# Kernel tuning notes

Measured on AMD Instinct MI355X. Metric: run time of the kernel, lower is better.

The kernel has to match this reference:

```python
import jax, jax.numpy as jnp
import numpy as np
import math

D_MODEL = 256
NUM_SLOTS = 128
RANK = 32
STEPS = 6
VOCAB = 32000
SEQ = 512
BATCH = 8
LN_EPS = 1e-5


def setup_inputs() -> dict:
    key = jax.random.key(0)
    ks = jax.random.split(key, 16)
    std = 0.02
    inp = {
        "input_ids": jax.random.randint(ks[0], (BATCH, SEQ), 0, VOCAB),
        "attention_mask": jnp.ones((BATCH, SEQ), dtype=jnp.int32),
        "token_emb": jax.random.normal(ks[1], (VOCAB, D_MODEL), jnp.float32) * std,
        "pos_emb": jax.random.normal(ks[2], (SEQ, D_MODEL), jnp.float32) * std,
        "H": jax.random.normal(ks[3], (NUM_SLOTS, D_MODEL), jnp.float32) / math.sqrt(D_MODEL),
        "W_source": jax.random.normal(ks[4], (NUM_SLOTS, NUM_SLOTS, D_MODEL, RANK), jnp.float32) * std,
        "W_target": jax.random.normal(ks[5], (NUM_SLOTS, NUM_SLOTS, RANK, D_MODEL), jnp.float32) * std,
        "Wq_in": jax.random.normal(ks[6], (D_MODEL, D_MODEL), jnp.float32) / math.sqrt(D_MODEL),
        "Wk_slots": jax.random.normal(ks[7], (D_MODEL, D_MODEL), jnp.float32) / math.sqrt(D_MODEL),
        "Wv_in": jax.random.normal(ks[8], (D_MODEL, D_MODEL), jnp.float32) / math.sqrt(D_MODEL),
        "Wq_out": jax.random.normal(ks[9], (D_MODEL, D_MODEL), jnp.float32) / math.sqrt(D_MODEL),
        "Wk_fin": jax.random.normal(ks[10], (D_MODEL, D_MODEL), jnp.float32) / math.sqrt(D_MODEL),
        "Wv_fin": jax.random.normal(ks[11], (D_MODEL, D_MODEL), jnp.float32) / math.sqrt(D_MODEL),
        "W_out_proj": jax.random.normal(ks[12], (VOCAB, D_MODEL), jnp.float32) / math.sqrt(D_MODEL),
        "ln_scale": jnp.ones((STEPS, D_MODEL), jnp.float32),
        "ln_bias": jnp.zeros((STEPS, D_MODEL), jnp.float32),
    }
    return inp


def _layernorm(x, g, b):
    mu = jnp.mean(x, axis=-1, keepdims=True)
    var = jnp.var(x, axis=-1, keepdims=True)
    return (x - mu) / jnp.sqrt(var + LN_EPS) * g + b


def _forward(input_ids, attention_mask, token_emb, pos_emb, H, W_source, W_target,
             Wq_in, Wk_slots, Wv_in, Wq_out, Wk_fin, Wv_fin, W_out_proj, ln_scale, ln_bias):
    B, L = input_ids.shape
    scale = 1.0 / math.sqrt(D_MODEL)
    # embeddings (dropout is identity in eval)
    X = token_emb[input_ids] + pos_emb[jnp.arange(L)][None]  # (B,L,D)
    # compress: input tokens -> slots
    Q_in = X @ Wq_in.T                      # (B,L,D)
    K_sl = H @ Wk_slots.T                   # (S,D)
    V_in = X @ Wv_in.T                      # (B,L,D)
    A = jax.nn.softmax(Q_in @ K_sl.T * scale, axis=-1)  # (B,L,S)
    m = attention_mask.astype(A.dtype)[..., None]
    A = A * m
    A = A / (jnp.sum(A, axis=1, keepdims=True) + 1e-8)
    IR = jnp.einsum('bls,bld->bsd', A, V_in)            # (B,S,D)
    H_state = H[None] + IR                               # (B,S,D)

    off_diag = (1.0 - jnp.eye(NUM_SLOTS, dtype=H_state.dtype))  # (S,S)

    def step(h, lnp):
        g, b = lnp
        # bilinear slot-to-slot influence; contract directly, no (B,S,S,D) expand of h
        inter = jnp.einsum('bid,ijdr->bijr', h, W_source)        # (B,S,S,R)
        out = jnp.einsum('bijr,ijrd->bijd', inter, W_target)     # (B,S,S,D)
        infl = jnp.einsum('bijd,ij->bjd', out, off_diag)         # mask diag + sum over i
        h = _layernorm(h + jax.nn.relu(infl), g, b)
        return h, None

    H_state, _ = jax.lax.scan(step, H_state, (ln_scale, ln_bias))

    # expand: slots -> tokens
    Q_out = X @ Wq_out.T                   # (B,L,D)
    K_f = H_state @ Wk_fin.T               # (B,S,D)
    V_f = H_state @ Wv_fin.T               # (B,S,D)
    A2 = jax.nn.softmax(jnp.einsum('bld,bsd->bls', Q_out, K_f) * scale, axis=-1)
    Y = jnp.einsum('bls,bsd->bld', A2, V_f)
    logits = Y @ W_out_proj.T              # (B,L,V)
    return logits


def reference(input_ids, attention_mask, token_emb, pos_emb, H, W_source, W_target,
              Wq_in, Wk_slots, Wv_in, Wq_out, Wk_fin, Wv_fin, W_out_proj, ln_scale, ln_bias):
    return _forward(input_ids, attention_mask, token_emb, pos_emb, H, W_source, W_target,
                    Wq_in, Wk_slots, Wv_in, Wq_out, Wk_fin, Wv_fin, W_out_proj, ln_scale, ln_bias)
```

## Files before the change

### kernel.cpp

```cpp
#include <hip/hip_runtime.h>
#include <hip/hip_bf16.h>
#include <math.h>

#define D_MODEL 256
#define NUM_SLOTS 128
#define RANK 32
#define N_STEPS 6
#define VOCAB 32000
#define SEQ 512
#define BATCH 8
#define NTOK (BATCH*SEQ)
#define LN_EPS 1e-5f
#define SM_SCALE 0.0625f
#define IGROUPS 8
#define IPG (NUM_SLOTS/IGROUPS)

typedef __attribute__((ext_vector_type(8))) short bf16x8;
typedef __attribute__((ext_vector_type(8))) _Float16 f16x8;
typedef __attribute__((ext_vector_type(4))) float f32x4;

#define GLD_LDS16(g, l) __builtin_amdgcn_global_load_lds( \
    (const __attribute__((address_space(1))) unsigned int*)(g), \
    (__attribute__((address_space(3))) unsigned int*)(l), 16, 0, 0)

__device__ inline unsigned pk2(float a, float b) {
    auto v = __builtin_amdgcn_cvt_pkrtz(a, b);
    union { decltype(v) x; unsigned u; } c;
    c.x = v;
    return c.u;
}
__device__ inline unsigned short f2h(float x) {
    union { _Float16 h; unsigned short u; } c;
    c.h = (_Float16)x;
    return c.u;
}

__global__ __launch_bounds__(256) void k_gemm_nt(const float* __restrict__ A,
        const float* __restrict__ B, float* __restrict__ C, int M, int N, int K) {
    __shared__ float As[32][64];
    __shared__ float Bs[32][64];
    int bm = blockIdx.x * 64, bn = blockIdx.y * 64;
    int t = threadIdx.x;
    int tm = (t & 15) * 4, tn = (t >> 4) * 4;
    float acc[4][4] = {};
    for (int k0 = 0; k0 < K; k0 += 32) {
        #pragma unroll
        for (int r = 0; r < 8; ++r) {
            int idx = r*256 + t;
            int m = idx >> 5, k = idx & 31;
            As[k][m] = A[(size_t)(bm+m)*K + k0 + k];
        }
        #pragma unroll
        for (int r = 0; r < 8; ++r) {
            int idx = r*256 + t;
            int n = idx >> 5, k = idx & 31;
            Bs[k][n] = B[(size_t)(bn+n)*K + k0 + k];
        }
        __syncthreads();
        #pragma unroll
        for (int k = 0; k < 32; ++k) {
            float4 a4 = *(const float4*)&As[k][tm];
            float4 b4 = *(const float4*)&Bs[k][tn];
            float a[4] = {a4.x,a4.y,a4.z,a4.w};
            float b[4] = {b4.x,b4.y,b4.z,b4.w};
            #pragma unroll
            for (int i = 0; i < 4; ++i)
                #pragma unroll
                for (int jj = 0; jj < 4; ++jj)
                    acc[i][jj] += a[i]*b[jj];
        }
        __syncthreads();
    }
    #pragma unroll
    for (int i = 0; i < 4; ++i) {
        float4 v = make_float4(acc[i][0],acc[i][1],acc[i][2],acc[i][3]);
        *(float4*)&C[(size_t)(bm+tm+i)*N + bn+tn] = v;
    }
}

__global__ __launch_bounds__(256) void k_gemm3e(const int* __restrict__ ids,
        const float* __restrict__ tok, const float* __restrict__ pos,
        const float* __restrict__ B0, const float* __restrict__ B1,
        const float* __restrict__ B2, float* __restrict__ C0,
        float* __restrict__ C1, float* __restrict__ C2) {
    const int K = D_MODEL, N = D_MODEL;
    const float* B = blockIdx.z == 0 ? B0 : (blockIdx.z == 1 ? B1 : B2);
    float* C = blockIdx.z == 0 ? C0 : (blockIdx.z == 1 ? C1 : C2);
    __shared__ float As[32][64];
    __shared__ float Bs[32][64];
    __shared__ int sid[64];
    int bm = blockIdx.x * 64, bn = blockIdx.y * 64;
    int t = threadIdx.x;
    if (t < 64) sid[t] = ids[bm + t];
    __syncthreads();
    int tm = (t & 15) * 4, tn = (t >> 4) * 4;
    float acc[4][4] = {};
    for (int k0 = 0; k0 < K; k0 += 32) {
        #pragma unroll
        for (int r = 0; r < 8; ++r) {
            int idx = r*256 + t;
            int m = idx >> 5, k = idx & 31;
            int gm = bm + m;
            As[k][m] = tok[(size_t)sid[m]*K + k0 + k] + pos[(gm & (SEQ-1))*K + k0 + k];
        }
        #pragma unroll
        for (int r = 0; r < 8; ++r) {
            int idx = r*256 + t;
            int n = idx >> 5, k = idx & 31;
            Bs[k][n] = B[(size_t)(bn+n)*K + k0 + k];
        }
        __syncthreads();
        #pragma unroll
        for (int k = 0; k < 32; ++k) {
            float4 a4 = *(const float4*)&As[k][tm];
            float4 b4 = *(const float4*)&Bs[k][tn];
            float a[4] = {a4.x,a4.y,a4.z,a4.w};
            float b[4] = {b4.x,b4.y,b4.z,b4.w};
            #pragma unroll
            for (int i = 0; i < 4; ++i)
                #pragma unroll
                for (int jj = 0; jj < 4; ++jj)
                    acc[i][jj] += a[i]*b[jj];
        }
        __syncthreads();
    }
    #pragma unroll
    for (int i = 0; i < 4; ++i) {
        float4 v = make_float4(acc[i][0],acc[i][1],acc[i][2],acc[i][3]);
        *(float4*)&C[(size_t)(bm+tm+i)*N + bn+tn] = v;
    }
}

__global__ __launch_bounds__(128) void k_attn1(const float* __restrict__ Qin,
        const float* __restrict__ Ksl, const int* __restrict__ mask,
        float* __restrict__ A) {
    int bl = blockIdx.x;
    int s = threadIdx.x;
    __shared__ float q[D_MODEL];
    __shared__ float red[128];
    q[s]       = Qin[(size_t)bl*D_MODEL + s];
    q[s + 128] = Qin[(size_t)bl*D_MODEL + s + 128];
    __syncthreads();
    const float* kr = Ksl + (size_t)s*D_MODEL;
    float acc = 0.f;
    #pragma unroll 8
    for (int d = 0; d < D_MODEL; ++d) acc += q[d]*kr[d];
    acc *= SM_SCALE;
    red[s] = acc; __syncthreads();
    for (int o = 64; o > 0; o >>= 1) { if (s < o) red[s] = fmaxf(red[s], red[s+o]); __syncthreads(); }
    float mx = red[0]; __syncthreads();
    float e = expf(acc - mx);
    red[s] = e; __syncthreads();
    for (int o = 64; o > 0; o >>= 1) { if (s < o) red[s] += red[s+o]; __syncthreads(); }
    float sum = red[0];
    float m = (float)mask[bl];
    A[(size_t)bl*NUM_SLOTS + s] = e / sum * m;
}

__global__ __launch_bounds__(256) void k_split16(const float* __restrict__ in,
        unsigned short* __restrict__ o, int n4) {
    int i = blockIdx.x*256 + threadIdx.x;
    if (i >= n4) return;
    float4 v = ((const float4*)in)[i];
    ushort4 h;
    h.x = f2h(v.x); h.y = f2h(v.y); h.z = f2h(v.z); h.w = f2h(v.w);
    ((ushort4*)o)[i] = h;
}

__global__ __launch_bounds__(256) void k_logits(
        const unsigned short* __restrict__ Ahg,
        const unsigned short* __restrict__ Bhg, float* __restrict__ C) {
    __shared__ unsigned short lds[2*8192];
    int bm = blockIdx.x * 128, bn = blockIdx.y * 128;
    int t = threadIdx.x;
    int w = t >> 6, l = t & 63;
    int wr = w >> 1, wc = w & 1;
    int lr = l & 15, lk = l >> 4;
    f32x4 acc[4][4];
    #pragma unroll
    for (int mi = 0; mi < 4; ++mi)
        #pragma unroll
        for (int ni = 0; ni < 4; ++ni)
            acc[mi][ni] = (f32x4){0.f,0.f,0.f,0.f};

    for (int kc = 0; kc < 4; ++kc) {
        if (kc) __syncthreads();
        #pragma unroll
        for (int i = 0; i < 4; ++i) {
            int c = t + i*256;
            int row = c >> 3, c8 = c & 7;
            size_t ga = (size_t)(bm+row)*256 + kc*64 + c8*8;
            size_t gb = (size_t)(bn+row)*256 + kc*64 + c8*8;
            GLD_LDS16(Ahg + ga, &lds[c*8]);
            GLD_LDS16(Bhg + gb, &lds[8192 + c*8]);
        }
        __syncthreads();
        #pragma unroll
        for (int s = 0; s < 2; ++s) {
            f16x8 ah[4], bh[4];
            #pragma unroll
            for (int mi = 0; mi < 4; ++mi) {
                int off = (wr*64 + mi*16 + lr)*64 + s*32 + lk*8;
                ah[mi] = *(const f16x8*)&lds[off];
            }
            #pragma unroll
            for (int ni = 0; ni < 4; ++ni) {
                int off = (wc*64 + ni*16 + lr)*64 + s*32 + lk*8;
                bh[ni] = *(const f16x8*)&lds[8192 + off];
            }
            #pragma unroll
            for (int mi = 0; mi < 4; ++mi)
                #pragma unroll
                for (int ni = 0; ni < 4; ++ni)
                    acc[mi][ni] = __builtin_amdgcn_mfma_f32_16x16x32_f16(ah[mi], bh[ni], acc[mi][ni], 0, 0, 0);
        }
    }
    #pragma unroll
    for (int mi = 0; mi < 4; ++mi)
        #pragma unroll
        for (int ni = 0; ni < 4; ++ni) {
            int col = bn + wc*64 + ni*16 + lr;
            #pragma unroll
            for (int r = 0; r < 4; ++r) {
                int row = bm + wr*64 + mi*16 + lk*4 + r;
                C[(size_t)row*VOCAB + col] = acc[mi][ni][r];
            }
        }
}

__global__ __launch_bounds__(256) void k_ir(const float* __restrict__ A,
        const float* __restrict__ V, const float* __restrict__ H,
        float* __restrict__ Hs, unsigned short* __restrict__ Hs16) {
    int bs = blockIdx.x; int b = bs >> 7; int s = bs & 127;
    int d = threadIdx.x;
    const float* Ab = A + (size_t)b*SEQ*NUM_SLOTS + s;
    const float* Vb = V + (size_t)b*SEQ*D_MODEL + d;
    float a0 = 0.f, a1 = 0.f, a2 = 0.f, a3 = 0.f;
    float s0 = 0.f, s1 = 0.f, s2 = 0.f, s3 = 0.f;
    for (int l = 0; l < SEQ; l += 4) {
        float w0 = Ab[(size_t)(l+0)*NUM_SLOTS];
        float w1 = Ab[(size_t)(l+1)*NUM_SLOTS];
        float w2 = Ab[(size_t)(l+2)*NUM_SLOTS];
        float w3 = Ab[(size_t)(l+3)*NUM_SLOTS];
        a0 += w0 * Vb[(size_t)(l+0)*D_MODEL];
        a1 += w1 * Vb[(size_t)(l+1)*D_MODEL];
        a2 += w2 * Vb[(size_t)(l+2)*D_MODEL];
        a3 += w3 * Vb[(size_t)(l+3)*D_MODEL];
        s0 += w0; s1 += w1; s2 += w2; s3 += w3;
    }
    float asum = (s0+s1) + (s2+s3) + 1e-8f;
    float acc = (a0+a1) + (a2+a3);
    float v = H[s*D_MODEL + d] + acc / asum;
    Hs[(size_t)bs*D_MODEL + d] = v;
    Hs16[(size_t)bs*D_MODEL + d] = f2h(v);
}

__global__ __launch_bounds__(256) void k_convert(const float* __restrict__ Ws,
        const float* __restrict__ Wt, unsigned short* __restrict__ WF) {
    int i = blockIdx.x, j = blockIdx.y, z = blockIdx.z;
    int t = threadIdx.x, w = t >> 6, l = t & 63;
    __shared__ float lds[4*1056];
    float* lw = &lds[w*1056];
    size_t sBase = ((size_t)i*128 + j)*8192;
    size_t pOut = ((size_t)j*128 + i)*16384;
    int g = l >> 4, c = l & 15;
    if (z < 2) {
        int ks = z*4 + w;
        const float4* s4 = (const float4*)(Ws + sBase) + ks*256;
        #pragma unroll
        for (int q = 0; q < 4; ++q) {
            int idx = q*64 + l;
            float4 v = s4[idx];
            *(float4*)&lw[(idx>>3)*33 + 4*(idx&7)] = v;
        }
        asm volatile("s_waitcnt lgkmcnt(0)" ::: "memory");
        bool diag = (i == j);
        #pragma unroll
        for (int mt = 0; mt < 2; ++mt) {
            union { f16x8 v; } o;
            #pragma unroll
            for (int e = 0; e < 8; ++e) {
                float f = diag ? 0.f : lw[(g*8 + e)*33 + mt*16 + c];
                o.v[e] = (_Float16)f;
            }
            *(f16x8*)(WF + pOut + (size_t)((ks*2 + mt)*64 + l)*8) = o.v;
        }
    } else {
        int p0 = (z - 2)*8 + w*2;
        const float4* s4 = (const float4*)(Wt + sBase);
        #pragma unroll
        for (int q = 0; q < 4; ++q) {
            int idx = q*64 + l;
            int r = idx >> 3, c8 = idx & 7;
            float4 v = s4[r*64 + p0*4 + c8];
            *(float4*)&lw[r*33 + 4*c8] = v;
        }
        asm volatile("s_waitcnt lgkmcnt(0)" ::: "memory");
        #pragma unroll
        for (int dn = 0; dn < 2; ++dn) {
            int nt = p0 + dn;
            union { f16x8 v; } o;
            #pragma unroll
            for (int e = 0; e < 8; ++e)
                o.v[e] = (_Float16)lw[(g*8 + e)*33 + dn*16 + c];
            *(f16x8*)(WF + pOut + 8192 + (size_t)(nt*64 + l)*8) = o.v;
        }
    }
}

__global__ __launch_bounds__(256, 4) void k_pairs_mfma(const unsigned short* __restrict__ h16,
        const unsigned short* __restrict__ WF, float* __restrict__ part) {
    __shared__ unsigned short lds[2*10240];
    int j = blockIdx.x, g = blockIdx.y;
    int t = threadIdx.x, w = t >> 6, l = t & 63;
    int lg = l >> 4, c = l & 15;
    const unsigned short* pbase = WF + ((size_t)j*128 + g*16)*16384;

    {
        const unsigned short* src = pbase;
        #pragma unroll
        for (int q = 0; q < 4; ++q)
            GLD_LDS16(src + (size_t)(q*256 + t)*8, &lds[(q*256 + t)*8]);
        const unsigned short* hsrc = h16 + ((size_t)(t&7)*NUM_SLOTS + g*16)*D_MODEL + (t>>3)*8;
        GLD_LDS16(hsrc, &lds[8192 + t*8]);
    }
    __builtin_amdgcn_sched_barrier(0);
    f16x8 bqn[4];
    #pragma unroll
    for (int nt = 0; nt < 4; ++nt)
        bqn[nt] = *(const f16x8*)(pbase + 8192 + (size_t)((w*4+nt)*64 + l)*8);
    __builtin_amdgcn_sched_barrier(0);

    f32x4 acc[4];
    #pragma unroll
    for (int nt = 0; nt < 4; ++nt) acc[nt] = (f32x4){0.f,0.f,0.f,0.f};
    f16x8 hzero;
    #pragma unroll
    for (int e = 0; e < 8; ++e) hzero[e] = (_Float16)0.f;

    #pragma unroll 2
    for (int ii = 0; ii < 16; ++ii) {
        int cur = ii & 1;
        asm volatile("s_waitcnt vmcnt(4) lgkmcnt(0)" ::: "memory");
        __builtin_amdgcn_s_barrier();
        __builtin_amdgcn_sched_barrier(0);
        if (ii < 15) {
            const unsigned short* src = pbase + (size_t)(ii+1)*16384;
            unsigned short* dst = &lds[(cur^1)*10240];
            #pragma unroll
            for (int q = 0; q < 4; ++q)
                GLD_LDS16(src + (size_t)(q*256 + t)*8, dst + (size_t)(q*256 + t)*8);
            const unsigned short* hsrc = h16 + ((size_t)(t&7)*NUM_SLOTS + (g*16+ii+1))*D_MODEL + (t>>3)*8;
            GLD_LDS16(hsrc, dst + 8192 + (size_t)t*8);
        }
        __builtin_amdgcn_sched_barrier(0);
        f16x8 bq[4];
        #pragma unroll
        for (int nt = 0; nt < 4; ++nt) bq[nt] = bqn[nt];
        if (ii < 15) {
            const unsigned short* bp = pbase + (size_t)(ii+1)*16384 + 8192;
            #pragma unroll
            for (int nt = 0; nt < 4; ++nt)
                bqn[nt] = *(const f16x8*)(bp + (size_t)((w*4+nt)*64 + l)*8);
        }
        const unsigned short* buf = &lds[cur*10240];
        f32x4 d1[2];
        d1[0] = (f32x4){0.f,0.f,0.f,0.f};
        d1[1] = (f32x4){0.f,0.f,0.f,0.f};
        #pragma unroll
        for (int ks = 0; ks < 8; ++ks) {
            f16x8 a0 = *(const f16x8*)(buf + (size_t)((ks*2+0)*64 + l)*8);
            f16x8 a1 = *(const f16x8*)(buf + (size_t)((ks*2+1)*64 + l)*8);
            f16x8 hv = *(const f16x8*)(buf + 8192 + (size_t)(((ks*4+lg)*8 + (c&7)))*8);
            f16x8 hb = (c < 8) ? hv : hzero;
            d1[0] = __builtin_amdgcn_mfma_f32_16x16x32_f16(a0, hb, d1[0], 0, 0, 0);
            d1[1] = __builtin_amdgcn_mfma_f32_16x16x32_f16(a1, hb, d1[1], 0, 0, 0);
        }
        unsigned q0 = pk2(d1[0][0], d1[0][1]);
        unsigned q1 = pk2(d1[0][2], d1[0][3]);
        unsigned s0 = pk2(d1[1][0], d1[1][1]);
        unsigned s1 = pk2(d1[1][2], d1[1][3]);
        int srcLo = 32*(lg & 1) + c;
        int srcHi = srcLo + 16;
        unsigned a0s = (unsigned)__shfl((int)q0, srcLo, 64);
        unsigned a1s = (unsigned)__shfl((int)q1, srcLo, 64);
        unsigned a2s = (unsigned)__shfl((int)q0, srcHi, 64);
        unsigned a3s = (unsigned)__shfl((int)q1, srcHi, 64);
        unsigned b0s = (unsigned)__shfl((int)s0, srcLo, 64);
        unsigned b1s = (unsigned)__shfl((int)s1, srcLo, 64);
        unsigned b2s = (unsigned)__shfl((int)s0, srcHi, 64);
        unsigned b3s = (unsigned)__shfl((int)s1, srcHi, 64);
        bool himt = ((lg >> 1) & 1);
        union { unsigned u[4]; f16x8 v; } A2u;
        A2u.u[0] = himt ? b0s : a0s;
        A2u.u[1] = himt ? b1s : a1s;
        A2u.u[2] = himt ? b2s : a2s;
        A2u.u[3] = himt ? b3s : a3s;
        #pragma unroll
        for (int nt = 0; nt < 4; ++nt)
            acc[nt] = __builtin_amdgcn_mfma_f32_16x16x32_f16(A2u.v, bq[nt], acc[nt], 0, 0, 0);
    }
    if (lg < 2) {
        #pragma unroll
        for (int nt = 0; nt < 4; ++nt) {
            int d = (w*4 + nt)*16 + c;
            #pragma unroll
            for (int r = 0; r < 4; ++r) {
                int b = lg*4 + r;
                part[(((size_t)g*BATCH + b)*NUM_SLOTS + j)*D_MODEL + d] = acc[nt][r];
            }
        }
    }
}

__global__ __launch_bounds__(256) void k_ln(float* __restrict__ h,
        unsigned short* __restrict__ h16, const float* __restrict__ part,
        const float* __restrict__ gma, const float* __restrict__ bta) {
    int bj = blockIdx.x;
    int t = threadIdx.x;
    int b = bj >> 7, j = bj & 127;
    __shared__ float red[256];
    float v = 0.f;
    #pragma unroll
    for (int g = 0; g < IGROUPS; ++g)
        v += part[(((size_t)g*BATCH + b)*NUM_SLOTS + j)*D_MODEL + t];
    float x = h[(size_t)bj*D_MODEL + t] + fmaxf(v, 0.f);
    red[t] = x; __syncthreads();
    for (int o = 128; o > 0; o >>= 1) { if (t < o) red[t] += red[t+o]; __syncthreads(); }
    float mu = red[0] * (1.0f/D_MODEL); __syncthreads();
    float dx = x - mu;
    red[t] = dx*dx; __syncthreads();
    for (int o = 128; o > 0; o >>= 1) { if (t < o) red[t] += red[t+o]; __syncthreads(); }
    float var = red[0] * (1.0f/D_MODEL);
    float outv = dx * rsqrtf(var + LN_EPS) * gma[t] + bta[t];
    h[(size_t)bj*D_MODEL + t] = outv;
    h16[(size_t)bj*D_MODEL + t] = f2h(outv);
}

__global__ __launch_bounds__(256) void k_kfvf(const float* __restrict__ A,
        const float* __restrict__ B0, const float* __restrict__ B1,
        float* __restrict__ C0, float* __restrict__ C1) {
    const int K = D_MODEL, N = D_MODEL;
    const float* B = blockIdx.z == 0 ? B0 : B1;
    float* C = blockIdx.z == 0 ? C0 : C1;
    __shared__ float As[32][64];
    __shared__ float Bs[32][64];
    int bm = blockIdx.x * 64, bn = blockIdx.y * 64;
    int t = threadIdx.x;
    int tm = (t & 15) * 4, tn = (t >> 4) * 4;
    float acc[4][4] = {};
    for (int k0 = 0; k0 < K; k0 += 32) {
        #pragma unroll
        for (int r = 0; r < 8; ++r) {
            int idx = r*256 + t;
            int m = idx >> 5, k = idx & 31;
            As[k][m] = A[(size_t)(bm+m)*K + k0 + k];
        }
        #pragma unroll
        for (int r = 0; r < 8; ++r) {
            int idx = r*256 + t;
            int n = idx >> 5, k = idx & 31;
            Bs[k][n] = B[(size_t)(bn+n)*K + k0 + k];
        }
        __syncthreads();
        #pragma unroll
        for (int k = 0; k < 32; ++k) {
            float4 a4 = *(const float4*)&As[k][tm];
            float4 b4 = *(const float4*)&Bs[k][tn];
            float a[4] = {a4.x,a4.y,a4.z,a4.w};
            float b[4] = {b4.x,b4.y,b4.z,b4.w};
            #pragma unroll
            for (int i = 0; i < 4; ++i)
                #pragma unroll
                for (int jj = 0; jj < 4; ++jj)
                    acc[i][jj] += a[i]*b[jj];
        }
        __syncthreads();
    }
    #pragma unroll
    for (int i = 0; i < 4; ++i) {
        float4 v = make_float4(acc[i][0],acc[i][1],acc[i][2],acc[i][3]);
        *(float4*)&C[(size_t)(bm+tm+i)*N + bn+tn] = v;
    }
}

__global__ __launch_bounds__(256) void k_attn2y(const float* __restrict__ Q,
        const float* __restrict__ Kf, const float* __restrict__ Vf,
        unsigned short* __restrict__ Yh) {
    int bl = blockIdx.x; int b = bl / SEQ;
    int t = threadIdx.x;
    __shared__ float q[D_MODEL];
    __shared__ float prt[2][128];
    __shared__ float a[128];
    __shared__ float red[128];
    q[t] = Q[(size_t)bl*D_MODEL + t];
    __syncthreads();
    int s = t & 127, hf = t >> 7;
    const float* kf = Kf + ((size_t)b*NUM_SLOTS + s)*D_MODEL + hf*128;
    float accp = 0.f;
    #pragma unroll 8
    for (int d = 0; d < 128; ++d) accp += q[hf*128 + d]*kf[d];
    prt[hf][s] = accp;
    __syncthreads();
    float v = 0.f;
    if (t < 128) { v = (prt[0][t] + prt[1][t]) * SM_SCALE; red[t] = v; }
    __syncthreads();
    for (int o = 64; o > 0; o >>= 1) { if (t < o) red[t] = fmaxf(red[t], red[t+o]); __syncthreads(); }
    float mx = red[0]; __syncthreads();
    if (t < 128) { float e = expf(v - mx); a[t] = e; red[t] = e; }
    __syncthreads();
    for (int o = 64; o > 0; o >>= 1) { if (t < o) red[t] += red[t+o]; __syncthreads(); }
    float inv = 1.0f / red[0];
    __syncthreads();
    const float* vf = Vf + (size_t)b*NUM_SLOTS*D_MODEL + t;
    float y0 = 0.f, y1 = 0.f, y2 = 0.f, y3 = 0.f;
    #pragma unroll
    for (int s2 = 0; s2 < NUM_SLOTS; s2 += 4) {
        y0 += a[s2+0]*vf[(size_t)(s2+0)*D_MODEL];
        y1 += a[s2+1]*vf[(size_t)(s2+1)*D_MODEL];
        y2 += a[s2+2]*vf[(size_t)(s2+2)*D_MODEL];
        y3 += a[s2+3]*vf[(size_t)(s2+3)*D_MODEL];
    }
    float y = ((y0+y1) + (y2+y3)) * inv;
    Yh[(size_t)bl*D_MODEL + t] = f2h(y);
}

extern "C" void kernel_launch(void* const* d_in, const int* in_sizes, int n_in,
                              void* d_out, int out_size, void* d_ws, size_t ws_size,
                              hipStream_t stream) {
    const int*   ids    = (const int*)d_in[0];
    const int*   amask  = (const int*)d_in[1];
    const float* tok    = (const float*)d_in[2];
    const float* pos    = (const float*)d_in[3];
    const float* Hin    = (const float*)d_in[4];
    const float* Ws     = (const float*)d_in[5];
    const float* Wt     = (const float*)d_in[6];
    const float* Wq_in  = (const float*)d_in[7];
    const float* Wk_sl  = (const float*)d_in[8];
    const float* Wv_in  = (const float*)d_in[9];
    const float* Wq_out = (const float*)d_in[10];
    const float* Wk_fin = (const float*)d_in[11];
    const float* Wv_fin = (const float*)d_in[12];
    const float* Wop    = (const float*)d_in[13];
    const float* lnsc   = (const float*)d_in[14];
    const float* lnbs   = (const float*)d_in[15];
    float* out = (float*)d_out;

    const size_t WF_USH = (size_t)16384 * 16384;
    unsigned short* WF = (unsigned short*)d_ws;
    float* ws = (float*)(WF + WF_USH);

    float* X    = ws;
    float* Qin  = X    + (size_t)NTOK*D_MODEL;
    float* Vin  = Qin  + (size_t)NTOK*D_MODEL;
    float* Ksl  = Vin  + (size_t)NTOK*D_MODEL;
    float* Asc  = Ksl  + (size_t)NUM_SLOTS*D_MODEL;
    float* csp  = Asc  + (size_t)NTOK*NUM_SLOTS;
    float* Hst  = csp  + (size_t)BATCH*8*NUM_SLOTS;
    float* part = Hst  + (size_t)BATCH*NUM_SLOTS*D_MODEL;
    float* Qout = part + (size_t)IGROUPS*BATCH*NUM_SLOTS*D_MODEL;
    float* Kf   = Qout + (size_t)NTOK*D_MODEL;
    float* Vf   = Kf   + (size_t)BATCH*NUM_SLOTS*D_MODEL;
    float* A2   = Vf   + (size_t)BATCH*NUM_SLOTS*D_MODEL;
    float* Yb   = A2   + (size_t)NTOK*NUM_SLOTS;
    unsigned short* Yh = (unsigned short*)(Yb + (size_t)NTOK*D_MODEL);
    unsigned short* Yl = Yh + (size_t)NTOK*D_MODEL;
    unsigned short* Wf16 = Yl + (size_t)NTOK*D_MODEL;
    unsigned short* Hst16 = Wf16 + (size_t)VOCAB*D_MODEL;

    k_convert<<<dim3(128, 128, 4), 256, 0, stream>>>(Ws, Wt, WF);
    k_split16<<<(VOCAB*D_MODEL/4 + 255)/256, 256, 0, stream>>>(Wop, Wf16, VOCAB*D_MODEL/4);

    k_gemm3e<<<dim3(NTOK/64, 4, 3), 256, 0, stream>>>(ids, tok, pos,
            Wq_in, Wv_in, Wq_out, Qin, Vin, Qout);
    k_gemm_nt<<<dim3(2, 4), 256, 0, stream>>>(Hin, Wk_sl, Ksl, NUM_SLOTS, D_MODEL, D_MODEL);
    k_attn1<<<NTOK, 128, 0, stream>>>(Qin, Ksl, amask, Asc);
    k_ir<<<BATCH*NUM_SLOTS, 256, 0, stream>>>(Asc, Vin, Hin, Hst, Hst16);
    for (int st = 0; st < N_STEPS; ++st) {
        k_pairs_mfma<<<dim3(NUM_SLOTS, IGROUPS), 256, 0, stream>>>(Hst16, WF, part);
        k_ln<<<BATCH*NUM_SLOTS, 256, 0, stream>>>(Hst, Hst16, part, lnsc + st*D_MODEL, lnbs + st*D_MODEL);
    }
    k_kfvf<<<dim3(BATCH*NUM_SLOTS/64, 4, 2), 256, 0, stream>>>(Hst, Wk_fin, Wv_fin, Kf, Vf);
    k_attn2y<<<NTOK, 256, 0, stream>>>(Qout, Kf, Vf, Yh);
    k_logits<<<dim3(NTOK/128, VOCAB/128), 256, 0, stream>>>(Yh, Wf16, out);
}
```

Before: 1.423 ms.

## Fuse front-end kernels with pair-weight conversion blocks to overlap independent work

The large W_source/W_target fp16 conversion and the W_out_proj split are no longer separate launches. Their blocks are appended to the front-end kernels (QKV projection, slot key GEMM, slot attention, slot aggregation), so the bandwidth-bound conversion runs alongside the small dependent front-end stages. This aims to fill idle CUs during those small kernels and remove launch gaps. The slot attention kernel also now uses 256 threads that split the dot product in half. In exchange the front kernels carry extra branching and a larger shared footprint, and the conversion is split across four launches that must add up to the full 65536 blocks.

```diff
diff --git a/kernel.cpp b/kernel.cpp
--- a/kernel.cpp
+++ b/kernel.cpp
@@ -13,7 +13,15 @@
 #define LN_EPS 1e-5f
 #define SM_SCALE 0.0625f
 #define IGROUPS 8
-#define IPG (NUM_SLOTS/IGROUPS)
+
+#define CB_A 0
+#define NC_A 15360
+#define CB_B (CB_A + NC_A)
+#define NC_B 11776
+#define CB_C (CB_B + NC_B)
+#define NC_C 19200
+#define CB_D (CB_C + NC_C)
+#define NC_D 19200
 
 typedef __attribute__((ext_vector_type(8))) short bf16x8;
 typedef __attribute__((ext_vector_type(8))) _Float16 f16x8;
@@ -35,12 +43,81 @@
     return c.u;
 }
 
-__global__ __launch_bounds__(256) void k_gemm_nt(const float* __restrict__ A,
-        const float* __restrict__ B, float* __restrict__ C, int M, int N, int K) {
-    __shared__ float As[32][64];
-    __shared__ float Bs[32][64];
-    int bm = blockIdx.x * 64, bn = blockIdx.y * 64;
-    int t = threadIdx.x;
+__device__ __forceinline__ void dev_convert(int cb, int t, float* ldsAll,
+        const float* __restrict__ Ws, const float* __restrict__ Wt,
+        unsigned short* __restrict__ WF) {
+    int z = cb >> 14, i = (cb >> 7) & 127, j = cb & 127;
+    int w = t >> 6, l = t & 63;
+    float* lw = &ldsAll[w*1056];
+    size_t sBase = ((size_t)i*128 + j)*8192;
+    size_t pOut = ((size_t)j*128 + i)*16384;
+    int g = l >> 4, c = l & 15;
+    if (z < 2) {
+        int ks = z*4 + w;
+        const float4* s4 = (const float4*)(Ws + sBase) + ks*256;
+        #pragma unroll
+        for (int q = 0; q < 4; ++q) {
+            int idx = q*64 + l;
+            float4 v = s4[idx];
+            *(float4*)&lw[(idx>>3)*33 + 4*(idx&7)] = v;
+        }
+        asm volatile("s_waitcnt lgkmcnt(0)" ::: "memory");
+        bool diag = (i == j);
+        #pragma unroll
+        for (int mt = 0; mt < 2; ++mt) {
+            union { f16x8 v; } o;
+            #pragma unroll
+            for (int e = 0; e < 8; ++e) {
+                float f = diag ? 0.f : lw[(g*8 + e)*33 + mt*16 + c];
+                o.v[e] = (_Float16)f;
+            }
+            *(f16x8*)(WF + pOut + (size_t)((ks*2 + mt)*64 + l)*8) = o.v;
+        }
+    } else {
+        int p0 = (z - 2)*8 + w*2;
+        const float4* s4 = (const float4*)(Wt + sBase);
+        #pragma unroll
+        for (int q = 0; q < 4; ++q) {
+            int idx = q*64 + l;
+            int r = idx >> 3, c8 = idx & 7;
+            float4 v = s4[r*64 + p0*4 + c8];
+            *(float4*)&lw[r*33 + 4*c8] = v;
+        }
+        asm volatile("s_waitcnt lgkmcnt(0)" ::: "memory");
+        #pragma unroll
+        for (int dn = 0; dn < 2; ++dn) {
+            int nt = p0 + dn;
+            union { f16x8 v; } o;
+            #pragma unroll
+            for (int e = 0; e < 8; ++e)
+                o.v[e] = (_Float16)lw[(g*8 + e)*33 + dn*16 + c];
+            *(f16x8*)(WF + pOut + 8192 + (size_t)(nt*64 + l)*8) = o.v;
+        }
+    }
+}
+
+__global__ __launch_bounds__(256) void k_front_a(const int* __restrict__ ids,
+        const float* __restrict__ tok, const float* __restrict__ pos,
+        const float* __restrict__ B0, const float* __restrict__ B1,
+        const float* __restrict__ B2, float* __restrict__ C0,
+        float* __restrict__ C1, float* __restrict__ C2,
+        const float* __restrict__ Ws, const float* __restrict__ Wt,
+        unsigned short* __restrict__ WF) {
+    __shared__ float smem[4352];
+    int bid = blockIdx.x;
+    int t = threadIdx.x;
+    if (bid >= 768) { dev_convert(CB_A + bid - 768, t, smem, Ws, Wt, WF); return; }
+    const int K = D_MODEL, N = D_MODEL;
+    int bx = bid & 63, byz = bid >> 6;
+    int by = byz & 3, bz = byz >> 2;
+    const float* B = bz == 0 ? B0 : (bz == 1 ? B1 : B2);
+    float* C = bz == 0 ? C0 : (bz == 1 ? C1 : C2);
+    float* As = smem;
+    float* Bs = smem + 2048;
+    int* sid = (int*)(smem + 4096);
+    int bm = bx * 64, bn = by * 64;
+    if (t < 64) sid[t] = ids[bm + t];
+    __syncthreads();
     int tm = (t & 15) * 4, tn = (t >> 4) * 4;
     float acc[4][4] = {};
     for (int k0 = 0; k0 < K; k0 += 32) {
@@ -48,19 +125,20 @@
         for (int r = 0; r < 8; ++r) {
             int idx = r*256 + t;
             int m = idx >> 5, k = idx & 31;
-            As[k][m] = A[(size_t)(bm+m)*K + k0 + k];
+            int gm = bm + m;
+            As[k*64 + m] = tok[(size_t)sid[m]*K + k0 + k] + pos[(gm & (SEQ-1))*K + k0 + k];
         }
         #pragma unroll
         for (int r = 0; r < 8; ++r) {
             int idx = r*256 + t;
             int n = idx >> 5, k = idx & 31;
-            Bs[k][n] = B[(size_t)(bn+n)*K + k0 + k];
+            Bs[k*64 + n] = B[(size_t)(bn+n)*K + k0 + k];
         }
         __syncthreads();
         #pragma unroll
         for (int k = 0; k < 32; ++k) {
-            float4 a4 = *(const float4*)&As[k][tm];
-            float4 b4 = *(const float4*)&Bs[k][tn];
+            float4 a4 = *(const float4*)&As[k*64 + tm];
+            float4 b4 = *(const float4*)&Bs[k*64 + tn];
             float a[4] = {a4.x,a4.y,a4.z,a4.w};
             float b[4] = {b4.x,b4.y,b4.z,b4.w};
             #pragma unroll
@@ -78,21 +156,28 @@
     }
 }
 
-__global__ __launch_bounds__(256) void k_gemm3e(const int* __restrict__ ids,
-        const float* __restrict__ tok, const float* __restrict__ pos,
-        const float* __restrict__ B0, const float* __restrict__ B1,
-        const float* __restrict__ B2, float* __restrict__ C0,
-        float* __restrict__ C1, float* __restrict__ C2) {
+__global__ __launch_bounds__(256) void k_front_b(const float* __restrict__ Hin,
+        const float* __restrict__ Wk_sl, float* __restrict__ Ksl,
+        const float* __restrict__ Wop, unsigned short* __restrict__ Wf16,
+        const float* __restrict__ Ws, const float* __restrict__ Wt,
+        unsigned short* __restrict__ WF) {
+    __shared__ float smem[4352];
+    int bid = blockIdx.x;
+    int t = threadIdx.x;
+    if (bid >= 8008) { dev_convert(CB_B + bid - 8008, t, smem, Ws, Wt, WF); return; }
+    if (bid >= 8) {
+        int i = (bid - 8)*256 + t;
+        float4 v = ((const float4*)Wop)[i];
+        ushort4 h;
+        h.x = f2h(v.x); h.y = f2h(v.y); h.z = f2h(v.z); h.w = f2h(v.w);
+        ((ushort4*)Wf16)[i] = h;
+        return;
+    }
     const int K = D_MODEL, N = D_MODEL;
-    const float* B = blockIdx.z == 0 ? B0 : (blockIdx.z == 1 ? B1 : B2);
-    float* C = blockIdx.z == 0 ? C0 : (blockIdx.z == 1 ? C1 : C2);
-    __shared__ float As[32][64];
-    __shared__ float Bs[32][64];
-    __shared__ int sid[64];
-    int bm = blockIdx.x * 64, bn = blockIdx.y * 64;
-    int t = threadIdx.x;
-    if (t < 64) sid[t] = ids[bm + t];
-    __syncthreads();
+    int bx = bid & 1, by = bid >> 1;
+    float* As = smem;
+    float* Bs = smem + 2048;
+    int bm = bx * 64, bn = by * 64;
     int tm = (t & 15) * 4, tn = (t >> 4) * 4;
     float acc[4][4] = {};
     for (int k0 = 0; k0 < K; k0 += 32) {
@@ -100,20 +185,19 @@
         for (int r = 0; r < 8; ++r) {
             int idx = r*256 + t;
             int m = idx >> 5, k = idx & 31;
-            int gm = bm + m;
-            As[k][m] = tok[(size_t)sid[m]*K + k0 + k] + pos[(gm & (SEQ-1))*K + k0 + k];
+            As[k*64 + m] = Hin[(size_t)(bm+m)*K + k0 + k];
         }
         #pragma unroll
         for (int r = 0; r < 8; ++r) {
             int idx = r*256 + t;
             int n = idx >> 5, k = idx & 31;
-            Bs[k][n] = B[(size_t)(bn+n)*K + k0 + k];
+            Bs[k*64 + n] = Wk_sl[(size_t)(bn+n)*K + k0 + k];
         }
         __syncthreads();
         #pragma unroll
         for (int k = 0; k < 32; ++k) {
-            float4 a4 = *(const float4*)&As[k][tm];
-            float4 b4 = *(const float4*)&Bs[k][tn];
+            float4 a4 = *(const float4*)&As[k*64 + tm];
+            float4 b4 = *(const float4*)&Bs[k*64 + tn];
             float a[4] = {a4.x,a4.y,a4.z,a4.w};
             float b[4] = {b4.x,b4.y,b4.z,b4.w};
             #pragma unroll
@@ -127,112 +211,59 @@
     #pragma unroll
     for (int i = 0; i < 4; ++i) {
         float4 v = make_float4(acc[i][0],acc[i][1],acc[i][2],acc[i][3]);
-        *(float4*)&C[(size_t)(bm+tm+i)*N + bn+tn] = v;
-    }
-}
-
-__global__ __launch_bounds__(128) void k_attn1(const float* __restrict__ Qin,
+        *(float4*)&Ksl[(size_t)(bm+tm+i)*N + bn+tn] = v;
+    }
+}
+
+__global__ __launch_bounds__(256) void k_front_c(const float* __restrict__ Qin,
         const float* __restrict__ Ksl, const int* __restrict__ mask,
-        float* __restrict__ A) {
-    int bl = blockIdx.x;
-    int s = threadIdx.x;
-    __shared__ float q[D_MODEL];
-    __shared__ float red[128];
-    q[s]       = Qin[(size_t)bl*D_MODEL + s];
-    q[s + 128] = Qin[(size_t)bl*D_MODEL + s + 128];
-    __syncthreads();
-    const float* kr = Ksl + (size_t)s*D_MODEL;
-    float acc = 0.f;
+        float* __restrict__ A,
+        const float* __restrict__ Ws, const float* __restrict__ Wt,
+        unsigned short* __restrict__ WF) {
+    __shared__ float smem[4352];
+    int bid = blockIdx.x;
+    int t = threadIdx.x;
+    if (bid >= NTOK) { dev_convert(CB_C + bid - NTOK, t, smem, Ws, Wt, WF); return; }
+    int bl = bid;
+    float* q   = smem;
+    float* prt = smem + 256;
+    float* red = smem + 512;
+    q[t] = Qin[(size_t)bl*D_MODEL + t];
+    __syncthreads();
+    int s = t & 127, hf = t >> 7;
+    const float* kr = Ksl + (size_t)s*D_MODEL + hf*128;
+    float accp = 0.f;
     #pragma unroll 8
-    for (int d = 0; d < D_MODEL; ++d) acc += q[d]*kr[d];
-    acc *= SM_SCALE;
-    red[s] = acc; __syncthreads();
-    for (int o = 64; o > 0; o >>= 1) { if (s < o) red[s] = fmaxf(red[s], red[s+o]); __syncthreads(); }
+    for (int d = 0; d < 128; ++d) accp += q[hf*128 + d]*kr[d];
+    prt[hf*128 + s] = accp;
+    __syncthreads();
+    float v = 0.f;
+    if (t < 128) { v = (prt[t] + prt[128 + t]) * SM_SCALE; red[t] = v; }
+    __syncthreads();
+    for (int o = 64; o > 0; o >>= 1) { if (t < o) red[t] = fmaxf(red[t], red[t+o]); __syncthreads(); }
     float mx = red[0]; __syncthreads();
-    float e = expf(acc - mx);
-    red[s] = e; __syncthreads();
-    for (int o = 64; o > 0; o >>= 1) { if (s < o) red[s] += red[s+o]; __syncthreads(); }
+    float e = 0.f;
+    if (t < 128) { e = expf(v - mx); red[t] = e; }
+    __syncthreads();
+    for (int o = 64; o > 0; o >>= 1) { if (t < o) red[t] += red[t+o]; __syncthreads(); }
     float sum = red[0];
-    float m = (float)mask[bl];
-    A[(size_t)bl*NUM_SLOTS + s] = e / sum * m;
-}
-
-__global__ __launch_bounds__(256) void k_split16(const float* __restrict__ in,
-        unsigned short* __restrict__ o, int n4) {
-    int i = blockIdx.x*256 + threadIdx.x;
-    if (i >= n4) return;
-    float4 v = ((const float4*)in)[i];
-    ushort4 h;
-    h.x = f2h(v.x); h.y = f2h(v.y); h.z = f2h(v.z); h.w = f2h(v.w);
-    ((ushort4*)o)[i] = h;
-}
-
-__global__ __launch_bounds__(256) void k_logits(
-        const unsigned short* __restrict__ Ahg,
-        const unsigned short* __restrict__ Bhg, float* __restrict__ C) {
-    __shared__ unsigned short lds[2*8192];
-    int bm = blockIdx.x * 128, bn = blockIdx.y * 128;
-    int t = threadIdx.x;
-    int w = t >> 6, l = t & 63;
-    int wr = w >> 1, wc = w & 1;
-    int lr = l & 15, lk = l >> 4;
-    f32x4 acc[4][4];
-    #pragma unroll
-    for (int mi = 0; mi < 4; ++mi)
-        #pragma unroll
-        for (int ni = 0; ni < 4; ++ni)
-            acc[mi][ni] = (f32x4){0.f,0.f,0.f,0.f};
-
-    for (int kc = 0; kc < 4; ++kc) {
-        if (kc) __syncthreads();
-        #pragma unroll
-        for (int i = 0; i < 4; ++i) {
-            int c = t + i*256;
-            int row = c >> 3, c8 = c & 7;
-            size_t ga = (size_t)(bm+row)*256 + kc*64 + c8*8;
-            size_t gb = (size_t)(bn+row)*256 + kc*64 + c8*8;
-            GLD_LDS16(Ahg + ga, &lds[c*8]);
-            GLD_LDS16(Bhg + gb, &lds[8192 + c*8]);
-        }
-        __syncthreads();
-        #pragma unroll
-        for (int s = 0; s < 2; ++s) {
-            f16x8 ah[4], bh[4];
-            #pragma unroll
-            for (int mi = 0; mi < 4; ++mi) {
-                int off = (wr*64 + mi*16 + lr)*64 + s*32 + lk*8;
-                ah[mi] = *(const f16x8*)&lds[off];
-            }
-            #pragma unroll
-            for (int ni = 0; ni < 4; ++ni) {
-                int off = (wc*64 + ni*16 + lr)*64 + s*32 + lk*8;
-                bh[ni] = *(const f16x8*)&lds[8192 + off];
-            }
-            #pragma unroll
-            for (int mi = 0; mi < 4; ++mi)
-                #pragma unroll
-                for (int ni = 0; ni < 4; ++ni)
-                    acc[mi][ni] = __builtin_amdgcn_mfma_f32_16x16x32_f16(ah[mi], bh[ni], acc[mi][ni], 0, 0, 0);
-        }
-    }
-    #pragma unroll
-    for (int mi = 0; mi < 4; ++mi)
-        #pragma unroll
-        for (int ni = 0; ni < 4; ++ni) {
-            int col = bn + wc*64 + ni*16 + lr;
-            #pragma unroll
-            for (int r = 0; r < 4; ++r) {
-                int row = bm + wr*64 + mi*16 + lk*4 + r;
-                C[(size_t)row*VOCAB + col] = acc[mi][ni][r];
-            }
-        }
-}
-
-__global__ __launch_bounds__(256) void k_ir(const float* __restrict__ A,
+    if (t < 128) {
+        float m = (float)mask[bl];
+        A[(size_t)bl*NUM_SLOTS + t] = e / sum * m;
+    }
+}
+
+__global__ __launch_bounds__(256) void k_front_d(const float* __restrict__ A,
         const float* __restrict__ V, const float* __restrict__ H,
-        float* __restrict__ Hs, unsigned short* __restrict__ Hs16) {
-    int bs = blockIdx.x; int b = bs >> 7; int s = bs & 127;
-    int d = threadIdx.x;
+        float* __restrict__ Hs, unsigned short* __restrict__ Hs16,
+        const float* __restrict__ Ws, const float* __restrict__ Wt,
+        unsigned short* __restrict__ WF) {
+    __shared__ float smem[4352];
+    int bid = blockIdx.x;
+    int t = threadIdx.x;
+    if (bid >= BATCH*NUM_SLOTS) { dev_convert(CB_D + bid - BATCH*NUM_SLOTS, t, smem, Ws, Wt, WF); return; }
+    int bs = bid; int b = bs >> 7; int s = bs & 127;
+    int d = t;
     const float* Ab = A + (size_t)b*SEQ*NUM_SLOTS + s;
     const float* Vb = V + (size_t)b*SEQ*D_MODEL + d;
     float a0 = 0.f, a1 = 0.f, a2 = 0.f, a3 = 0.f;
@@ -255,57 +286,65 @@
     Hs16[(size_t)bs*D_MODEL + d] = f2h(v);
 }
 
-__global__ __launch_bounds__(256) void k_convert(const float* __restrict__ Ws,
-        const float* __restrict__ Wt, unsigned short* __restrict__ WF) {
-    int i = blockIdx.x, j = blockIdx.y, z = blockIdx.z;
-    int t = threadIdx.x, w = t >> 6, l = t & 63;
-    __shared__ float lds[4*1056];
-    float* lw = &lds[w*1056];
-    size_t sBase = ((size_t)i*128 + j)*8192;
-    size_t pOut = ((size_t)j*128 + i)*16384;
-    int g = l >> 4, c = l & 15;
-    if (z < 2) {
-        int ks = z*4 + w;
-        const float4* s4 = (const float4*)(Ws + sBase) + ks*256;
-        #pragma unroll
-        for (int q = 0; q < 4; ++q) {
-            int idx = q*64 + l;
-            float4 v = s4[idx];
-            *(float4*)&lw[(idx>>3)*33 + 4*(idx&7)] = v;
-        }
-        asm volatile("s_waitcnt lgkmcnt(0)" ::: "memory");
-        bool diag = (i == j);
-        #pragma unroll
-        for (int mt = 0; mt < 2; ++mt) {
-            union { f16x8 v; } o;
-            #pragma unroll
-            for (int e = 0; e < 8; ++e) {
-                float f = diag ? 0.f : lw[(g*8 + e)*33 + mt*16 + c];
-                o.v[e] = (_Float16)f;
+__global__ __launch_bounds__(256) void k_logits(
+        const unsigned short* __restrict__ Ahg,
+        const unsigned short* __restrict__ Bhg, float* __restrict__ C) {
+    __shared__ unsigned short lds[2*8192];
+    int bm = blockIdx.x * 128, bn = blockIdx.y * 128;
+    int t = threadIdx.x;
+    int w = t >> 6, l = t & 63;
+    int wr = w >> 1, wc = w & 1;
+    int lr = l & 15, lk = l >> 4;
+    f32x4 acc[4][4];
+    #pragma unroll
+    for (int mi = 0; mi < 4; ++mi)
+        #pragma unroll
+        for (int ni = 0; ni < 4; ++ni)
+            acc[mi][ni] = (f32x4){0.f,0.f,0.f,0.f};
+
+    for (int kc = 0; kc < 4; ++kc) {
+        if (kc) __syncthreads();
+        #pragma unroll
+        for (int i = 0; i < 4; ++i) {
+            int c = t + i*256;
+            int row = c >> 3, c8 = c & 7;
+            size_t ga = (size_t)(bm+row)*256 + kc*64 + c8*8;
+            size_t gb = (size_t)(bn+row)*256 + kc*64 + c8*8;
+            GLD_LDS16(Ahg + ga, &lds[c*8]);
+            GLD_LDS16(Bhg + gb, &lds[8192 + c*8]);
+        }
+        __syncthreads();
+        #pragma unroll
+        for (int s = 0; s < 2; ++s) {
+            f16x8 ah[4], bh[4];
+            #pragma unroll
+            for (int mi = 0; mi < 4; ++mi) {
+                int off = (wr*64 + mi*16 + lr)*64 + s*32 + lk*8;
+                ah[mi] = *(const f16x8*)&lds[off];
             }
-            *(f16x8*)(WF + pOut + (size_t)((ks*2 + mt)*64 + l)*8) = o.v;
-        }
-    } else {
-        int p0 = (z - 2)*8 + w*2;
-        const float4* s4 = (const float4*)(Wt + sBase);
-        #pragma unroll
-        for (int q = 0; q < 4; ++q) {
-            int idx = q*64 + l;
-            int r = idx >> 3, c8 = idx & 7;
-            float4 v = s4[r*64 + p0*4 + c8];
-            *(float4*)&lw[r*33 + 4*c8] = v;
-        }
-        asm volatile("s_waitcnt lgkmcnt(0)" ::: "memory");
-        #pragma unroll
-        for (int dn = 0; dn < 2; ++dn) {
-            int nt = p0 + dn;
-            union { f16x8 v; } o;
-            #pragma unroll
-            for (int e = 0; e < 8; ++e)
-                o.v[e] = (_Float16)lw[(g*8 + e)*33 + dn*16 + c];
-            *(f16x8*)(WF + pOut + 8192 + (size_t)(nt*64 + l)*8) = o.v;
-        }
-    }
+            #pragma unroll
+            for (int ni = 0; ni < 4; ++ni) {
+                int off = (wc*64 + ni*16 + lr)*64 + s*32 + lk*8;
+                bh[ni] = *(const f16x8*)&lds[8192 + off];
+            }
+            #pragma unroll
+            for (int mi = 0; mi < 4; ++mi)
+                #pragma unroll
+                for (int ni = 0; ni < 4; ++ni)
+                    acc[mi][ni] = __builtin_amdgcn_mfma_f32_16x16x32_f16(ah[mi], bh[ni], acc[mi][ni], 0, 0, 0);
+        }
+    }
+    #pragma unroll
+    for (int mi = 0; mi < 4; ++mi)
+        #pragma unroll
+        for (int ni = 0; ni < 4; ++ni) {
+            int col = bn + wc*64 + ni*16 + lr;
+            #pragma unroll
+            for (int r = 0; r < 4; ++r) {
+                int row = bm + wr*64 + mi*16 + lk*4 + r;
+                C[(size_t)row*VOCAB + col] = acc[mi][ni][r];
+            }
+        }
 }
 
 __global__ __launch_bounds__(256, 4) void k_pairs_mfma(const unsigned short* __restrict__ h16,
@@ -568,14 +607,12 @@
     unsigned short* Wf16 = Yl + (size_t)NTOK*D_MODEL;
     unsigned short* Hst16 = Wf16 + (size_t)VOCAB*D_MODEL;
 
-    k_convert<<<dim3(128, 128, 4), 256, 0, stream>>>(Ws, Wt, WF);
-    k_split16<<<(VOCAB*D_MODEL/4 + 255)/256, 256, 0, stream>>>(Wop, Wf16, VOCAB*D_MODEL/4);
-
-    k_gemm3e<<<dim3(NTOK/64, 4, 3), 256, 0, stream>>>(ids, tok, pos,
-            Wq_in, Wv_in, Wq_out, Qin, Vin, Qout);
-    k_gemm_nt<<<dim3(2, 4), 256, 0, stream>>>(Hin, Wk_sl, Ksl, NUM_SLOTS, D_MODEL, D_MODEL);
-    k_attn1<<<NTOK, 128, 0, stream>>>(Qin, Ksl, amask, Asc);
-    k_ir<<<BATCH*NUM_SLOTS, 256, 0, stream>>>(Asc, Vin, Hin, Hst, Hst16);
+    k_front_a<<<768 + NC_A, 256, 0, stream>>>(ids, tok, pos,
+            Wq_in, Wv_in, Wq_out, Qin, Vin, Qout, Ws, Wt, WF);
+    k_front_b<<<8008 + NC_B, 256, 0, stream>>>(Hin, Wk_sl, Ksl, Wop, Wf16, Ws, Wt, WF);
+    k_front_c<<<NTOK + NC_C, 256, 0, stream>>>(Qin, Ksl, amask, Asc, Ws, Wt, WF);
+    k_front_d<<<BATCH*NUM_SLOTS + NC_D, 256, 0, stream>>>(Asc, Vin, Hin, Hst, Hst16, Ws, Wt, WF);
+
     for (int st = 0; st < N_STEPS; ++st) {
         k_pairs_mfma<<<dim3(NUM_SLOTS, IGROUPS), 256, 0, stream>>>(Hst16, WF, part);
         k_ln<<<BATCH*NUM_SLOTS, 256, 0, stream>>>(Hst, Hst16, part, lnsc + st*D_MODEL, lnbs + st*D_MODEL);
```

New measurement: 1.352 ms (median of 2 runs). 1.05x faster.
